# Kernel tuning notes

Measured on AMD Instinct MI355X. Metric: run time of the kernel, lower is better.

The kernel has to match this reference:

```python
import jax, jax.numpy as jnp
import numpy as np
from jax import lax

SQRT2 = 1.4142135623730951
SCALE_BOUND = 0.11
LIK_BOUND = 1e-9

def conv2d(x, w, b, pad):
    y = lax.conv_general_dilated(x, w, (1, 1), [(pad, pad), (pad, pad)],
                                 dimension_numbers=('NCHW', 'OIHW', 'NCHW'))
    return y + b[None, :, None, None]

def space_to_depth(x):  # pixel_unshuffle, block=2: [B,C,H,W]->[B,4C,H/2,W/2]
    B, C, H, W = x.shape
    x = x.reshape(B, C, H // 2, 2, W // 2, 2)
    return x.transpose(0, 1, 3, 5, 2, 4).reshape(B, 4 * C, H // 2, W // 2)

def lrelu(x):
    return jnp.where(x >= 0, x, 0.01 * x)

def gauss_cdf(x):
    return 0.5 * (1.0 + lax.erf(x / SQRT2))

def setup_inputs() -> dict:
    key = jax.random.key(0)
    ks = jax.random.split(key, 6)
    B, F_, P, H, W = 4, 128, 128, 256, 256
    inp = {
        'input': jax.random.normal(ks[0], (B, F_, H, W), jnp.float32) * 2.0,
        'condition': jax.random.normal(ks[1], (B, P // 4, H, W), jnp.float32),
        'lstm_w': jax.random.normal(ks[2], (4 * P, F_ + P, 3, 3), jnp.float32) * 0.02,
        'lstm_b': jnp.zeros((4 * P,), jnp.float32),
        'w1': jax.random.normal(ks[3], (2 * F_, P + F_, 1, 1), jnp.float32) * 0.05,
        'b1': jnp.zeros((2 * F_,), jnp.float32),
        'w2': jax.random.normal(ks[4], (2 * F_, 2 * F_, 3, 3), jnp.float32) * 0.02,
        'b2': jnp.zeros((2 * F_,), jnp.float32),
        'w3': jax.random.normal(ks[5], (2 * F_, 2 * F_, 1, 1), jnp.float32) * 0.05,
        'b3': jnp.zeros((2 * F_,), jnp.float32),
    }
    return inp

def reference(input, condition, lstm_w, lstm_b, w1, b1, w2, b2, w3, b3):
    # quantize (round with straight-through estimator, as in trc quant)
    q = input + lax.stop_gradient(jnp.round(input) - input)
    y = space_to_depth(q)                       # [B,4F,h,w]
    groups = jnp.split(y, 4, axis=1)
    if condition.shape[-2:] == input.shape[-2:]:
        condition = space_to_depth(condition)   # [B,P,h,w]
    h = condition
    c = condition
    lls = []
    for g in range(4):
        yi = groups[g - 1] if g else jnp.zeros_like(groups[0])
        # ConvLSTM cell: single conv over [input, hidden] -> 4 gates
        gates = conv2d(jnp.concatenate([yi, h], axis=1), lstm_w, lstm_b, 1)
        i_g, f_g, o_g, g_g = jnp.split(gates, 4, axis=1)
        c = jax.nn.sigmoid(f_g) * c + jax.nn.sigmoid(i_g) * jnp.tanh(g_g)
        h = jax.nn.sigmoid(o_g) * jnp.tanh(c)
        # reparam stack -> (mean, scale) condition
        t = lrelu(conv2d(jnp.concatenate([h, yi], axis=1), w1, b1, 0))
        t = lrelu(conv2d(t, w2, b2, 1))
        cnd = conv2d(t, w3, b3, 0)
        mean, scale = jnp.split(cnd, 2, axis=1)
        scale = jnp.maximum(scale, SCALE_BOUND)
        z = groups[g]
        up = gauss_cdf((z - mean + 0.5) / scale)
        lo = gauss_cdf((z - mean - 0.5) / scale)
        lls.append(jnp.maximum(up - lo, LIK_BOUND))
    likelihood = jnp.concatenate(lls, axis=1)   # [B,4F,h,w]
    return q, likelihood
```

## Files before the change

kernel.cpp:

```cpp
#include <hip/hip_runtime.h>
#include <math.h>

typedef unsigned short u16;
typedef __attribute__((ext_vector_type(8))) short bf16x8;
typedef __attribute__((ext_vector_type(4))) float f32x4;

#define PSUB8 540800
#define TSUB8 524288

__device__ __forceinline__ u16 f2bf(float f) {
  unsigned u = __float_as_uint(f);
  unsigned r = u + 0x7fffu + ((u >> 16) & 1u);
  return (u16)(r >> 16);
}
__device__ __forceinline__ float bf2f(u16 h) {
  return __uint_as_float(((unsigned)h) << 16);
}
__device__ __forceinline__ void gl16(const u16* g, const u16* l) {
  __builtin_amdgcn_global_load_lds(
      (const __attribute__((address_space(1))) void*)g,
      (__attribute__((address_space(3))) void*)l, 16, 0, 0);
}
__device__ __forceinline__ float sigm_f(float x) {
  return __builtin_amdgcn_rcpf(1.f + __expf(-x));
}
__device__ __forceinline__ float tanh_f(float x) {
  float xc = fminf(fmaxf(x, -20.f), 20.f);
  float e = __expf(2.f * xc);
  return (e - 1.f) * __builtin_amdgcn_rcpf(e + 1.f);
}

__global__ void quant_s2d_kernel(const float* __restrict__ inp,
                                 float* __restrict__ q,
                                 u16* __restrict__ yghi) {
  int idx = blockIdx.x * 256 + threadIdx.x;
  int ww = idx & 255;
  int hh = (idx >> 8) & 255;
  int cc = (idx >> 16) & 127;
  int b  = idx >> 23;
  float v = rintf(inp[idx]);
  q[idx] = v;
  int g = cc >> 5;
  int f = ((cc & 31) << 2) | ((hh & 1) << 1) | (ww & 1);
  int y = hh >> 1, x = ww >> 1;
  int p = (b * 130 + y + 1) * 130 + 1 + x;
  yghi[((size_t)(g * 16 + (f >> 3))) * PSUB8 + (size_t)p * 8 + (f & 7)] = f2bf(v);
}

__global__ void s2d_cond_kernel(const float* __restrict__ cond,
                                u16* __restrict__ hhi, float* __restrict__ c0) {
  int idx = blockIdx.x * 256 + threadIdx.x;
  int ww = idx & 255;
  int hh = (idx >> 8) & 255;
  int cc = (idx >> 16) & 31;
  int b  = idx >> 21;
  float v = cond[idx];
  int ch = (cc << 2) | ((hh & 1) << 1) | (ww & 1);
  int y = hh >> 1, x = ww >> 1;
  int p = (b * 130 + y + 1) * 130 + 1 + x;
  hhi[(size_t)(ch >> 3) * PSUB8 + (size_t)p * 8 + (ch & 7)] = f2bf(v);
  c0[((size_t)(b * 128 + y) * 128 + x) * 128 + ch] = v;
}

__global__ void zero_halos(u16* __restrict__ base) {
  int e = blockIdx.x * 256 + threadIdx.x;
  if (e >= 516 * 8) return;
  int pb = blockIdx.y;
  int px = e >> 3, ch = e & 7;
  int y, x;
  if (px < 130)      { y = 0;            x = px; }
  else if (px < 260) { y = 129;          x = px - 130; }
  else if (px < 388) { y = px - 260 + 1; x = 0; }
  else               { y = px - 388 + 1; x = 129; }
  int plane = pb >> 2, b = pb & 3;
  base[(size_t)plane * PSUB8 + (size_t)((b * 130 + y) * 130 + x) * 8 + ch] = 0;
}

template <int TAPS, int PERM>
__global__ void build_wpack(const float* __restrict__ w, u16* __restrict__ o) {
  int idx = blockIdx.x * 256 + threadIdx.x;
  int jj = idx & 7, lane = (idx >> 3) & 63, ni = (idx >> 9) & 3, wn = (idx >> 11) & 1;
  int rest = idx >> 12;
  const int NSLAB = TAPS * 8;
  int slab = rest % NSLAB, cb = rest / NSLAB;
  int c = cb * 128 + wn * 64 + ni * 16 + (lane & 15);
  int k = slab * 32 + ((lane >> 4) << 3) + jj;
  int tap = (TAPS == 9) ? (k >> 8) : 0;
  int ci = (TAPS == 9) ? (k & 255) : k;
  int oc;
  if (PERM == 0)      oc = ((c >> 4) & 3) * 128 + (c >> 7) * 32 + ((c >> 6) & 1) * 16 + (c & 15);
  else if (PERM == 2) oc = ((c >> 4) & 1) * 128 + (c >> 7) * 64 + ((c >> 6) & 1) * 32 + ((c >> 5) & 1) * 16 + (c & 15);
  else                oc = c;
  float v = w[((size_t)(oc * 256 + ci)) * TAPS + tap];
  o[idx] = f2bf(v);
}

__global__ void make_biases(const float* __restrict__ lb, const float* __restrict__ b1,
                            const float* __restrict__ b2, const float* __restrict__ b3,
                            float* __restrict__ pl, float* __restrict__ p1,
                            float* __restrict__ p2, float* __restrict__ p3) {
  int t = blockIdx.x * 256 + threadIdx.x;
  if (t < 512) {
    int gate = (t >> 4) & 3;
    int f = (t >> 7) * 32 + ((t >> 6) & 1) * 16 + (t & 15);
    pl[t] = lb[gate * 128 + f];
  }
  if (t < 256) {
    p1[t] = b1[t];
    p2[t] = b2[t];
    int m = (t >> 4) & 1;
    int f = (t >> 7) * 64 + ((t >> 6) & 1) * 32 + ((t >> 5) & 1) * 16 + (t & 15);
    p3[t] = b3[m * 128 + f];
  }
}

template <int TAPS, int NCOL, int EPI, int SKIP>
__global__ __launch_bounds__(256, 4)
void conv_mfma(const u16* __restrict__ a0, const u16* __restrict__ a1,
               const u16* __restrict__ Wpk, const float* __restrict__ biasP,
               float* __restrict__ c_io,
               u16* __restrict__ ohi, size_t OSUB, int ORS, int OPAD,
               const u16* __restrict__ zsrc, float* __restrict__ lik, int g) {
  constexpr int NSLAB = TAPS * 8;
  constexpr int NS = SKIP ? NSLAB / 2 : NSLAB;
  constexpr int NCB = NCOL / 128;
  constexpr bool COMPACT = (EPI == 2);
  constexpr int RS = COMPACT ? 128 : 130;
  constexpr int PAD = COMPACT ? 0 : 1;
  constexpr size_t PST = COMPACT ? (size_t)TSUB8 : (size_t)PSUB8;
  __shared__ __attribute__((aligned(16))) u16 lds[16384];
  const int tid = threadIdx.x;
  const int lane = tid & 63, wid = tid >> 6;
  const int wm = wid >> 1, wn = wid & 1;
  const int fl = lane & 15, kq = lane >> 4;

  int n = blockIdx.y * NCB + blockIdx.x;
  int w_ = n >> 9, r_ = n & 511;
  int xj = r_ & 7, tt = r_ >> 3;
  const int cb = tt & (NCB - 1);
  const int YL = 64 / NCB;
  int ystrip = w_ * (8 * YL) + xj * YL + (tt / NCB);
  const int b = ystrip >> 7, y = ystrip & 127;

  f32x4 acc[4][4] = {};

  const int origin0 = (b * RS + y + PAD) * RS + PAD;
  const u16* a0w = a0 + (size_t)origin0 * 8 + (size_t)wid * PST;
  const u16* a1w = a1 + (size_t)origin0 * 8 + (size_t)wid * PST;
  const u16* Ww  = Wpk + (size_t)cb * NSLAB * 4096 + (size_t)wid * 1024 + (size_t)lane * 8;
  u16* ldsA = &lds[wid * 1024];
  u16* ldsW = &lds[8192 + wid * 1024];

  auto stage = [&](int si, int buf) {
    int ms;
    if (SKIP == 0) ms = si;
    else {
      int tp = si >> 2, o = si & 3;
      ms = tp * 8 + (SKIP == 1 ? 4 + o : o);
    }
    int cc = ms & 7;
    int tap = ms >> 3;
    int dy = (TAPS == 9) ? tap / 3 - 1 : 0;
    int dx = (TAPS == 9) ? tap % 3 - 1 : 0;
    const u16* aw = (cc < 4) ? a0w : a1w;
    long abase = (long)(cc & 3) * 4 * (long)PST + (long)(dy * RS + dx) * 8;
#pragma unroll
    for (int t = 0; t < 2; ++t)
      gl16(aw + abase + t * 512 + lane * 8, ldsA + buf * 4096 + t * 512);
#pragma unroll
    for (int t = 0; t < 2; ++t)
      gl16(Ww + (long)ms * 4096 + t * 512, ldsW + buf * 4096 + t * 512);
  };
  auto compute = [&](int buf) {
    bf16x8 Ah[4], Wf[4];
#pragma unroll
    for (int i = 0; i < 4; ++i)
      Ah[i] = *(const bf16x8*)&lds[buf * 4096 + kq * 1024 + (wm * 64 + i * 16 + fl) * 8];
#pragma unroll
    for (int i = 0; i < 4; ++i)
      Wf[i] = *(const bf16x8*)&lds[8192 + buf * 4096 + wn * 2048 + i * 512 + lane * 8];
    __builtin_amdgcn_s_setprio(1);
#pragma unroll
    for (int mi = 0; mi < 4; ++mi)
#pragma unroll
      for (int ni = 0; ni < 4; ++ni)
        acc[mi][ni] = __builtin_amdgcn_mfma_f32_16x16x32_bf16(Ah[mi], Wf[ni], acc[mi][ni], 0, 0, 0);
    __builtin_amdgcn_s_setprio(0);
  };

  stage(0, 0);
#pragma unroll
  for (int s = 0; s < NS; ++s) {
    if (s + 1 < NS) {
      stage(s + 1, (s + 1) & 1);
      asm volatile("s_waitcnt vmcnt(4)" ::: "memory");
    } else {
      asm volatile("s_waitcnt vmcnt(0)" ::: "memory");
    }
    __builtin_amdgcn_s_barrier();
    compute(s & 1);
    __builtin_amdgcn_s_barrier();
  }

  if (EPI == 0) {
    const int f = cb * 32 + wn * 16 + fl;
    float bi[4];
#pragma unroll
    for (int ni = 0; ni < 4; ++ni) bi[ni] = biasP[cb * 128 + wn * 64 + ni * 16 + fl];
#pragma unroll
    for (int mi = 0; mi < 4; ++mi)
#pragma unroll
      for (int r = 0; r < 4; ++r) {
        int x = wm * 64 + mi * 16 + kq * 4 + r;
        size_t ci = ((size_t)(b * 128 + y) * 128 + x) * 128 + f;
        float ig = sigm_f(acc[mi][0][r] + bi[0]);
        float fg = sigm_f(acc[mi][1][r] + bi[1]);
        float og = sigm_f(acc[mi][2][r] + bi[2]);
        float gg = tanh_f(acc[mi][3][r] + bi[3]);
        float cn = fg * c_io[ci] + ig * gg;
        c_io[ci] = cn;
        float hv = og * tanh_f(cn);
        size_t hx = (size_t)((b * 130 + y + 1) * 130 + 1 + x);
        ohi[(size_t)(f >> 3) * PSUB8 + hx * 8 + (f & 7)] = f2bf(hv);
      }
  } else if (EPI == 1) {
#pragma unroll
    for (int ni = 0; ni < 4; ++ni) {
      int c = cb * 128 + wn * 64 + ni * 16 + fl;
      float bv = biasP[c];
#pragma unroll
      for (int mi = 0; mi < 4; ++mi)
#pragma unroll
        for (int r = 0; r < 4; ++r) {
          int x = wm * 64 + mi * 16 + kq * 4 + r;
          float v = acc[mi][ni][r] + bv;
          v = (v >= 0.f) ? v : 0.01f * v;
          size_t op = (size_t)((b * ORS + y + OPAD) * ORS + OPAD + x);
          ohi[(size_t)(c >> 3) * OSUB + op * 8 + (c & 7)] = f2bf(v);
        }
    }
  } else {
#pragma unroll
    for (int j = 0; j < 2; ++j) {
      int f = cb * 64 + wn * 32 + j * 16 + fl;
      float bm = biasP[cb * 128 + wn * 64 + j * 32 + fl];
      float bs = biasP[cb * 128 + wn * 64 + j * 32 + 16 + fl];
#pragma unroll
      for (int mi = 0; mi < 4; ++mi)
#pragma unroll
        for (int r = 0; r < 4; ++r) {
          int x = wm * 64 + mi * 16 + kq * 4 + r;
          float mean = acc[mi][2 * j][r] + bm;
          float sc = fmaxf(acc[mi][2 * j + 1][r] + bs, 0.11f);
          size_t zp = (size_t)((b * 130 + y + 1) * 130 + 1 + x);
          float z = bf2f(zsrc[(size_t)(f >> 3) * PSUB8 + zp * 8 + (f & 7)]);
          float is = 0.70710678118654752f / sc;
          float up = 0.5f * (1.f + erff((z - mean + 0.5f) * is));
          float lo_ = 0.5f * (1.f + erff((z - mean - 0.5f) * is));
          lik[((size_t)(b * 512 + g * 128 + f) * 128 + y) * 128 + x] = fmaxf(up - lo_, 1e-9f);
        }
    }
  }
}

extern "C" void kernel_launch(void* const* d_in, const int* in_sizes, int n_in,
                              void* d_out, int out_size, void* d_ws, size_t ws_size,
                              hipStream_t stream) {
  const float* input  = (const float*)d_in[0];
  const float* cond   = (const float*)d_in[1];
  const float* lstm_w = (const float*)d_in[2];
  const float* lstm_b = (const float*)d_in[3];
  const float* w1 = (const float*)d_in[4];
  const float* b1 = (const float*)d_in[5];
  const float* w2 = (const float*)d_in[6];
  const float* b2 = (const float*)d_in[7];
  const float* w3 = (const float*)d_in[8];
  const float* b3 = (const float*)d_in[9];

  float* q   = (float*)d_out;
  float* lik = q + 33554432;

  char* ws = (char*)d_ws;
  u16* YG    = (u16*)(ws + 0);
  u16* HAhi  = (u16*)(ws + 69222400);
  u16* HBhi  = (u16*)(ws + 86528000);
  u16* T1hi  = (u16*)(ws + 103833600);
  u16* T2hi  = (u16*)(ws + 138444800);
  float* cbuf = (float*)(ws + 171999232);
  u16* WLpk = (u16*)(ws + 205553664);
  u16* W2pk = (u16*)(ws + 207912960);
  u16* W1pk = (u16*)(ws + 209092608);
  u16* W3pk = (u16*)(ws + 209223680);
  float* PL = (float*)(ws + 209354752);
  float* P1 = PL + 512;
  float* P2 = P1 + 256;
  float* P3 = P2 + 256;

  zero_halos<<<dim3(17, 512), 256, 0, stream>>>((u16*)ws);

  quant_s2d_kernel<<<131072, 256, 0, stream>>>(input, q, YG);
  s2d_cond_kernel<<<32768, 256, 0, stream>>>(cond, HAhi, cbuf);
  build_wpack<9, 0><<<4608, 256, 0, stream>>>(lstm_w, WLpk);
  build_wpack<9, 1><<<2304, 256, 0, stream>>>(w2, W2pk);
  build_wpack<1, 1><<<256, 256, 0, stream>>>(w1, W1pk);
  build_wpack<1, 2><<<256, 256, 0, stream>>>(w3, W3pk);
  make_biases<<<2, 256, 0, stream>>>(lstm_b, b1, b2, b3, PL, P1, P2, P3);

  for (int g = 0; g < 4; ++g) {
    u16* hinhi  = (g & 1) ? HBhi : HAhi;
    u16* houthi = (g & 1) ? HAhi : HBhi;
    const u16* yihi = g ? (YG + (size_t)(g - 1) * 16 * PSUB8) : hinhi;
    const u16* zg = YG + (size_t)g * 16 * PSUB8;

    if (g == 0) {
      conv_mfma<9, 512, 0, 1><<<dim3(4, 512), 256, 0, stream>>>(
          hinhi, hinhi, WLpk, PL, cbuf, houthi, PSUB8, 0, 0, nullptr, nullptr, g);
      conv_mfma<1, 256, 1, 2><<<dim3(2, 512), 256, 0, stream>>>(
          houthi, houthi, W1pk, P1, nullptr, T1hi, PSUB8, 130, 1, nullptr, nullptr, g);
    } else {
      conv_mfma<9, 512, 0, 0><<<dim3(4, 512), 256, 0, stream>>>(
          yihi, hinhi, WLpk, PL, cbuf, houthi, PSUB8, 0, 0, nullptr, nullptr, g);
      conv_mfma<1, 256, 1, 0><<<dim3(2, 512), 256, 0, stream>>>(
          houthi, yihi, W1pk, P1, nullptr, T1hi, PSUB8, 130, 1, nullptr, nullptr, g);
    }
    conv_mfma<9, 256, 1, 0><<<dim3(2, 512), 256, 0, stream>>>(
        T1hi, T1hi + (size_t)16 * PSUB8, W2pk, P2, nullptr, T2hi, TSUB8, 128, 0,
        nullptr, nullptr, g);
    conv_mfma<1, 256, 2, 0><<<dim3(2, 512), 256, 0, stream>>>(
        T2hi, T2hi + (size_t)16 * TSUB8, W3pk, P3, nullptr, nullptr, 0, 0, 0,
        zg, lik, g);
  }
}
```

Baseline: 1.179 ms.

## Load conv weights directly into registers and triple-buffer activation LDS tiles

The MFMA conv kernel stops staging weight slabs through LDS. Each wave now loads its B-fragments straight from global memory into registers, ping-ponging between two register sets. Activation slabs use a three-deep LDS ring, which allows one barrier per slab instead of two and shrinks LDS use to 24 KB. The aim is to cut LDS traffic and barrier stalls and to allow more resident blocks, at the cost of duplicated weight loads across waves that go through cache, plus higher register pressure.

```diff
diff --git a/kernel.cpp b/kernel.cpp
--- a/kernel.cpp
+++ b/kernel.cpp
@@ -128,7 +128,7 @@
   constexpr int RS = COMPACT ? 128 : 130;
   constexpr int PAD = COMPACT ? 0 : 1;
   constexpr size_t PST = COMPACT ? (size_t)TSUB8 : (size_t)PSUB8;
-  __shared__ __attribute__((aligned(16))) u16 lds[16384];
+  __shared__ __attribute__((aligned(16))) u16 lds[12288];
   const int tid = threadIdx.x;
   const int lane = tid & 63, wid = tid >> 6;
   const int wm = wid >> 1, wn = wid & 1;
@@ -147,59 +147,67 @@
   const int origin0 = (b * RS + y + PAD) * RS + PAD;
   const u16* a0w = a0 + (size_t)origin0 * 8 + (size_t)wid * PST;
   const u16* a1w = a1 + (size_t)origin0 * 8 + (size_t)wid * PST;
-  const u16* Ww  = Wpk + (size_t)cb * NSLAB * 4096 + (size_t)wid * 1024 + (size_t)lane * 8;
+  const bf16x8* Wroot = (const bf16x8*)Wpk + (size_t)cb * NSLAB * 512 + wn * 256 + lane;
   u16* ldsA = &lds[wid * 1024];
-  u16* ldsW = &lds[8192 + wid * 1024];
-
-  auto stage = [&](int si, int buf) {
-    int ms;
-    if (SKIP == 0) ms = si;
-    else {
-      int tp = si >> 2, o = si & 3;
-      ms = tp * 8 + (SKIP == 1 ? 4 + o : o);
-    }
+
+  auto mapslab = [&](int si) -> int {
+    if (SKIP == 0) return si;
+    int tp = si >> 2, o = si & 3;
+    return tp * 8 + (SKIP == 1 ? 4 + o : o);
+  };
+  auto issueA = [&](int si, int buf) {
+    int ms = mapslab(si);
     int cc = ms & 7;
     int tap = ms >> 3;
     int dy = (TAPS == 9) ? tap / 3 - 1 : 0;
     int dx = (TAPS == 9) ? tap % 3 - 1 : 0;
     const u16* aw = (cc < 4) ? a0w : a1w;
     long abase = (long)(cc & 3) * 4 * (long)PST + (long)(dy * RS + dx) * 8;
-#pragma unroll
-    for (int t = 0; t < 2; ++t)
-      gl16(aw + abase + t * 512 + lane * 8, ldsA + buf * 4096 + t * 512);
-#pragma unroll
-    for (int t = 0; t < 2; ++t)
-      gl16(Ww + (long)ms * 4096 + t * 512, ldsW + buf * 4096 + t * 512);
+    gl16(aw + abase + lane * 8,       ldsA + buf * 4096);
+    gl16(aw + abase + 512 + lane * 8, ldsA + buf * 4096 + 512);
   };
-  auto compute = [&](int buf) {
-    bf16x8 Ah[4], Wf[4];
+  auto issueW = [&](int si, bf16x8* W) {
+    int ms = mapslab(si);
+#pragma unroll
+    for (int i = 0; i < 4; ++i) W[i] = Wroot[(size_t)ms * 512 + i * 64];
+  };
+  auto compute = [&](const bf16x8* W, int buf) {
+    bf16x8 Ah[4];
 #pragma unroll
     for (int i = 0; i < 4; ++i)
       Ah[i] = *(const bf16x8*)&lds[buf * 4096 + kq * 1024 + (wm * 64 + i * 16 + fl) * 8];
-#pragma unroll
-    for (int i = 0; i < 4; ++i)
-      Wf[i] = *(const bf16x8*)&lds[8192 + buf * 4096 + wn * 2048 + i * 512 + lane * 8];
     __builtin_amdgcn_s_setprio(1);
 #pragma unroll
     for (int mi = 0; mi < 4; ++mi)
 #pragma unroll
       for (int ni = 0; ni < 4; ++ni)
-        acc[mi][ni] = __builtin_amdgcn_mfma_f32_16x16x32_bf16(Ah[mi], Wf[ni], acc[mi][ni], 0, 0, 0);
+        acc[mi][ni] = __builtin_amdgcn_mfma_f32_16x16x32_bf16(Ah[mi], W[ni], acc[mi][ni], 0, 0, 0);
     __builtin_amdgcn_s_setprio(0);
   };
 
-  stage(0, 0);
-#pragma unroll
-  for (int s = 0; s < NS; ++s) {
+  bf16x8 WA[4], WB[4];
+  issueA(0, 0);
+  issueW(0, WA);
+#pragma unroll
+  for (int s = 0; s < NS; s += 2) {
     if (s + 1 < NS) {
-      stage(s + 1, (s + 1) & 1);
-      asm volatile("s_waitcnt vmcnt(4)" ::: "memory");
+      issueW(s + 1, WB);
+      issueA(s + 1, (s + 1) % 3);
+      asm volatile("s_waitcnt vmcnt(6)" ::: "memory");
     } else {
       asm volatile("s_waitcnt vmcnt(0)" ::: "memory");
     }
     __builtin_amdgcn_s_barrier();
-    compute(s & 1);
+    compute(WA, s % 3);
+    if (s + 2 < NS) {
+      issueW(s + 2, WA);
+      issueA(s + 2, (s + 2) % 3);
+      asm volatile("s_waitcnt vmcnt(6)" ::: "memory");
+    } else {
+      asm volatile("s_waitcnt vmcnt(0)" ::: "memory");
+    }
     __builtin_amdgcn_s_barrier();
+    compute(WB, (s + 1) % 3);
   }
 
   if (EPI == 0) {
```

After: 1.232 ms. 1.05x slower.

## Triple-buffer activation tiles and use one barrier per K-step in conv MFMA loop

Applied to the files above, without the earlier changes.

Splits the staged loads into separate activation and weight issues. Activation slabs are prefetched two steps ahead into a three-deep LDS ring, while weights stay double-buffered and are prefetched one step ahead. The trailing barrier is dropped: the next loads are issued after the single barrier, right before compute, so memory latency overlaps more MFMA work. LDS per block grows from 32KB to 40KB, which could lower occupancy.

```diff
diff --git a/kernel.cpp b/kernel.cpp
--- a/kernel.cpp
+++ b/kernel.cpp
@@ -128,7 +128,7 @@
   constexpr int RS = COMPACT ? 128 : 130;
   constexpr int PAD = COMPACT ? 0 : 1;
   constexpr size_t PST = COMPACT ? (size_t)TSUB8 : (size_t)PSUB8;
-  __shared__ __attribute__((aligned(16))) u16 lds[16384];
+  __shared__ __attribute__((aligned(16))) u16 lds[20480];
   const int tid = threadIdx.x;
   const int lane = tid & 63, wid = tid >> 6;
   const int wm = wid >> 1, wn = wid & 1;
@@ -149,15 +149,15 @@
   const u16* a1w = a1 + (size_t)origin0 * 8 + (size_t)wid * PST;
   const u16* Ww  = Wpk + (size_t)cb * NSLAB * 4096 + (size_t)wid * 1024 + (size_t)lane * 8;
   u16* ldsA = &lds[wid * 1024];
-  u16* ldsW = &lds[8192 + wid * 1024];
-
-  auto stage = [&](int si, int buf) {
-    int ms;
-    if (SKIP == 0) ms = si;
-    else {
-      int tp = si >> 2, o = si & 3;
-      ms = tp * 8 + (SKIP == 1 ? 4 + o : o);
-    }
+  u16* ldsW = &lds[12288 + wid * 1024];
+
+  auto mapslab = [&](int si) -> int {
+    if (SKIP == 0) return si;
+    int tp = si >> 2, o = si & 3;
+    return tp * 8 + (SKIP == 1 ? 4 + o : o);
+  };
+  auto issueA = [&](int si, int buf) {
+    int ms = mapslab(si);
     int cc = ms & 7;
     int tap = ms >> 3;
     int dy = (TAPS == 9) ? tap / 3 - 1 : 0;
@@ -167,18 +167,21 @@
 #pragma unroll
     for (int t = 0; t < 2; ++t)
       gl16(aw + abase + t * 512 + lane * 8, ldsA + buf * 4096 + t * 512);
+  };
+  auto issueW = [&](int si, int buf) {
+    int ms = mapslab(si);
 #pragma unroll
     for (int t = 0; t < 2; ++t)
       gl16(Ww + (long)ms * 4096 + t * 512, ldsW + buf * 4096 + t * 512);
   };
-  auto compute = [&](int buf) {
+  auto compute = [&](int bufA, int bufW) {
     bf16x8 Ah[4], Wf[4];
 #pragma unroll
     for (int i = 0; i < 4; ++i)
-      Ah[i] = *(const bf16x8*)&lds[buf * 4096 + kq * 1024 + (wm * 64 + i * 16 + fl) * 8];
+      Ah[i] = *(const bf16x8*)&lds[bufA * 4096 + kq * 1024 + (wm * 64 + i * 16 + fl) * 8];
 #pragma unroll
     for (int i = 0; i < 4; ++i)
-      Wf[i] = *(const bf16x8*)&lds[8192 + buf * 4096 + wn * 2048 + i * 512 + lane * 8];
+      Wf[i] = *(const bf16x8*)&lds[12288 + bufW * 4096 + wn * 2048 + i * 512 + lane * 8];
     __builtin_amdgcn_s_setprio(1);
 #pragma unroll
     for (int mi = 0; mi < 4; ++mi)
@@ -188,18 +191,18 @@
     __builtin_amdgcn_s_setprio(0);
   };
 
-  stage(0, 0);
+  issueA(0, 0);
+  issueW(0, 0);
+  issueA(1, 1);
 #pragma unroll
   for (int s = 0; s < NS; ++s) {
-    if (s + 1 < NS) {
-      stage(s + 1, (s + 1) & 1);
-      asm volatile("s_waitcnt vmcnt(4)" ::: "memory");
-    } else {
-      asm volatile("s_waitcnt vmcnt(0)" ::: "memory");
-    }
+    if (s + 1 < NS) asm volatile("s_waitcnt vmcnt(2)" ::: "memory");
+    else            asm volatile("s_waitcnt vmcnt(0)" ::: "memory");
     __builtin_amdgcn_s_barrier();
-    compute(s & 1);
-    __builtin_amdgcn_s_barrier();
+    asm volatile("" ::: "memory");
+    if (s + 1 < NS) issueW(s + 1, (s + 1) & 1);
+    if (s + 2 < NS) issueA(s + 2, (s + 2) % 3);
+    compute(s % 3, s & 1);
   }
 
   if (EPI == 0) {
```

Result: no change. 1.181 ms (+0.2%).
